# Performance work log

Hardware: AMD Instinct MI355X
Metric: run time of the kernel (lower is better)

Reference implementation:

```python
import jax, jax.numpy as jnp
import numpy as np

NEG_INF = -1e30  # stand-in for float('-inf') that is safe under softmax


def setup_inputs() -> dict:
    key = jax.random.key(0)
    k1, k2, k3, k4 = jax.random.split(key, 4)
    B, T, C, H = 4, 4096, 1024, 128
    x = jax.random.normal(k1, (B, T, C), dtype=jnp.float32)
    # nn.Linear(n_emb, head_size, bias=False): store as [C, H] so y = x @ W
    Wk = jax.random.normal(k2, (C, H), dtype=jnp.float32) * (C ** -0.5)
    Wq = jax.random.normal(k3, (C, H), dtype=jnp.float32) * (C ** -0.5)
    Wv = jax.random.normal(k4, (C, H), dtype=jnp.float32) * (C ** -0.5)
    return {"x": x, "Wk": Wk, "Wq": Wq, "Wv": Wv}


def reference(x, Wk, Wq, Wv):
    B, T, C = x.shape
    k = x @ Wk  # [B, T, H]
    q = x @ Wq  # [B, T, H]
    v = x @ Wv  # [B, T, H]
    # Faithful to original: wei = k @ q^T, scaled by C**-0.5 (C = n_emb)
    wei = jnp.einsum('bih,bjh->bij', k, q) * (C ** -0.5)  # [B, T, T]
    causal = jnp.tril(jnp.ones((T, T), dtype=bool))
    wei = jnp.where(causal, wei, NEG_INF)
    wei = jax.nn.softmax(wei, axis=-1)
    out = jnp.einsum('bij,bjh->bih', wei, v)  # [B, T, H]
    return out
```

## Files before the change

### kernel.cpp

```cpp
#include <hip/hip_runtime.h>
#include <hip/hip_bf16.h>

#define T_SEQ 4096
#define NBATCH 4
#define C_EMB 1024
#define H_DIM 128
#define M_ROWS (NBATCH * T_SEQ)
#define SPLIT 4

typedef __bf16 bf16x8 __attribute__((ext_vector_type(8)));
typedef float  floatx4 __attribute__((ext_vector_type(4)));

__device__ __forceinline__ ushort f2bf(float f) {
    __hip_bfloat16 h = __float2bfloat16(f);
    return *reinterpret_cast<ushort*>(&h);
}
__device__ __forceinline__ float bf2f(ushort u) {
    unsigned int v = ((unsigned int)u) << 16;
    return *reinterpret_cast<float*>(&v);
}
__device__ __forceinline__ uint4 pack8(const float4& a, const float4& b) {
    __hip_bfloat162 h0 = __float22bfloat162_rn(make_float2(a.x, a.y));
    __hip_bfloat162 h1 = __float22bfloat162_rn(make_float2(a.z, a.w));
    __hip_bfloat162 h2 = __float22bfloat162_rn(make_float2(b.x, b.y));
    __hip_bfloat162 h3 = __float22bfloat162_rn(make_float2(b.z, b.w));
    uint4 r;
    r.x = *reinterpret_cast<unsigned int*>(&h0);
    r.y = *reinterpret_cast<unsigned int*>(&h1);
    r.z = *reinterpret_cast<unsigned int*>(&h2);
    r.w = *reinterpret_cast<unsigned int*>(&h3);
    return r;
}
__device__ __forceinline__ void gld16(const ushort* g, ushort* l) {
    __builtin_amdgcn_global_load_lds(
        (const __attribute__((address_space(1))) unsigned int*)(g),
        (__attribute__((address_space(3))) unsigned int*)(l),
        16, 0, 0);
}

__global__ __launch_bounds__(256) void transpose_w(
    const float* __restrict__ Wk, const float* __restrict__ Wq,
    const float* __restrict__ Wv, ushort* __restrict__ wt) {
    const int z = blockIdx.y;
    const float* W = (z == 0) ? Wk : (z == 1) ? Wq : Wv;
    ushort* Wtz = wt + (size_t)z * H_DIM * C_EMB;
    int linear = blockIdx.x * 256 + threadIdx.x;
    int n  = linear >> 7;
    int k0 = (linear & 127) << 3;
    ushort tmp[8];
#pragma unroll
    for (int j = 0; j < 8; ++j)
        tmp[j] = f2bf(W[(size_t)(k0 + j) * H_DIM + n]);
    uint4 pk;
    pk.x = (unsigned int)tmp[0] | ((unsigned int)tmp[1] << 16);
    pk.y = (unsigned int)tmp[2] | ((unsigned int)tmp[3] << 16);
    pk.z = (unsigned int)tmp[4] | ((unsigned int)tmp[5] << 16);
    pk.w = (unsigned int)tmp[6] | ((unsigned int)tmp[7] << 16);
    *reinterpret_cast<uint4*>(Wtz + (size_t)n * C_EMB + k0) = pk;
}

__global__ __launch_bounds__(512, 1) void qkv_gemm(
    const float* __restrict__ x, const ushort* __restrict__ wt,
    ushort* __restrict__ kqv) {
    const int m0 = blockIdx.x * 64;

    __shared__ ushort As[2][64 * 64];
    __shared__ ushort Bs[2][384 * 64];

    const int tid  = threadIdx.x;
    const int lane = tid & 63;
    const int wave = tid >> 6;
    const int l15  = lane & 15;
    const int quad = lane >> 4;
    const int mg   = (wave >> 1) * 16;
    const int nb   = (wave & 1) * 12;

    floatx4 acc[12];
#pragma unroll
    for (int nj = 0; nj < 12; ++nj) acc[nj] = floatx4{0.f, 0.f, 0.f, 0.f};

    const int ar = tid >> 3;
    const int ac = tid & 7;
    const int chp = ac ^ (ar & 7);
    const float* xrow = x + (size_t)(m0 + ar) * C_EMB + ac * 8;

    float4 xa = *reinterpret_cast<const float4*>(xrow);
    float4 xb = *reinterpret_cast<const float4*>(xrow + 4);
#pragma unroll
    for (int i = 0; i < 6; ++i) {
        int rbase = wave * 48 + i * 8;
        int row = rbase + (lane >> 3);
        int chg = (lane & 7) ^ (row & 7);
        gld16(wt + (size_t)row * C_EMB + chg * 8, Bs[0] + rbase * 64);
    }
    *reinterpret_cast<uint4*>(As[0] + ar * 64 + chp * 8) = pack8(xa, xb);
    __syncthreads();
    xa = *reinterpret_cast<const float4*>(xrow + 64);
    xb = *reinterpret_cast<const float4*>(xrow + 68);

    for (int kt = 0; kt < 16; ++kt) {
        const int cur = kt & 1;

        if (kt < 15) {
#pragma unroll
            for (int i = 0; i < 6; ++i) {
                int rbase = wave * 48 + i * 8;
                int row = rbase + (lane >> 3);
                int chg = (lane & 7) ^ (row & 7);
                gld16(wt + (size_t)row * C_EMB + (kt + 1) * 64 + chg * 8,
                      Bs[cur ^ 1] + rbase * 64);
            }
            *reinterpret_cast<uint4*>(As[cur ^ 1] + ar * 64 + chp * 8) = pack8(xa, xb);
        }
        if (kt < 14) {
            const float* nsrc = xrow + (kt + 2) * 64;
            xa = *reinterpret_cast<const float4*>(nsrc);
            xb = *reinterpret_cast<const float4*>(nsrc + 4);
        }

#pragma unroll
        for (int kk = 0; kk < 2; ++kk) {
            bf16x8 a = *reinterpret_cast<const bf16x8*>(
                As[cur] + (mg + l15) * 64 + ((4 * kk + quad) ^ (l15 & 7)) * 8);
#pragma unroll
            for (int nj = 0; nj < 12; ++nj) {
                int brow = (nb + nj) * 16 + l15;
                bf16x8 b = *reinterpret_cast<const bf16x8*>(
                    Bs[cur] + brow * 64 + ((4 * kk + quad) ^ (brow & 7)) * 8);
                acc[nj] = __builtin_amdgcn_mfma_f32_16x16x32_bf16(a, b, acc[nj], 0, 0, 0);
            }
        }

        __syncthreads();
    }

    const int rowb = m0 + mg + quad * 4;
#pragma unroll
    for (int nj = 0; nj < 12; ++nj) {
        int gcol = (nb + nj) * 16 + l15;
        int z = gcol >> 7;
        int cz = gcol & 127;
        if (z < 2) {
            const float scale = (z == 0) ? 0.03125f : 1.0f;
            ushort* outz = kqv + (size_t)z * M_ROWS * H_DIM;
#pragma unroll
            for (int r = 0; r < 4; ++r)
                outz[(size_t)(rowb + r) * H_DIM + cz] = f2bf(acc[nj][r] * scale);
        } else {
            ushort* vt = kqv + (size_t)2 * M_ROWS * H_DIM;
            int bb   = rowb >> 12;
            int tloc = rowb & (T_SEQ - 1);
            ushort4 pk;
            pk.x = f2bf(acc[nj][0]);
            pk.y = f2bf(acc[nj][1]);
            pk.z = f2bf(acc[nj][2]);
            pk.w = f2bf(acc[nj][3]);
            *reinterpret_cast<ushort4*>(
                vt + ((size_t)(bb * H_DIM + cz) << 12) + tloc) = pk;
        }
    }
}

#define P_STRIDE 72
__global__ __launch_bounds__(256, 3) void flash_chunk(
    const ushort* __restrict__ kqv, ushort* __restrict__ partO,
    float* __restrict__ partML) {
    const int it = blockIdx.x >> 2;
    const int c  = blockIdx.x & 3;
    if (c > it) return;
    const int b  = blockIdx.y;
    const int i0 = it * 64;

    const ushort* Qg = kqv + (size_t)b * T_SEQ * H_DIM;
    const ushort* Kg = kqv + (size_t)M_ROWS * H_DIM + (size_t)b * T_SEQ * H_DIM;
    const ushort* Vt = kqv + (size_t)2 * M_ROWS * H_DIM + (size_t)b * H_DIM * T_SEQ;

    __shared__ ushort Ks[64 * 128];
    __shared__ ushort Vs[128 * 64];
    __shared__ ushort Ps[4][16 * P_STRIDE];

    const int tid  = threadIdx.x;
    const int lane = tid & 63;
    const int wave = tid >> 6;
    const int l15  = lane & 15;
    const int quad = lane >> 4;

    bf16x8 q[4];
    {
        const ushort* qrow = Qg + (size_t)(i0 + wave * 16 + l15) * H_DIM + quad * 8;
#pragma unroll
        for (int kk = 0; kk < 4; ++kk)
            q[kk] = *reinterpret_cast<const bf16x8*>(qrow + kk * 32);
    }

    float m_i[4], l_i[4];
#pragma unroll
    for (int r = 0; r < 4; ++r) { m_i[r] = -1e30f; l_i[r] = 0.f; }
    floatx4 o[8];
#pragma unroll
    for (int nh = 0; nh < 8; ++nh) o[nh] = floatx4{0.f, 0.f, 0.f, 0.f};

    ushort* Pw = Ps[wave];

    for (int jt = c; jt <= it; jt += SPLIT) {
        const int j0 = jt * 64;
        __syncthreads();
#pragma unroll
        for (int i = 0; i < 4; ++i) {
            int row = wave * 16 + i * 4 + (lane >> 4);
            int chg = (lane & 15) ^ (row & 15);
            gld16(Kg + (size_t)(j0 + row) * H_DIM + chg * 8,
                  Ks + (wave * 16 + i * 4) * 128);
        }
#pragma unroll
        for (int i = 0; i < 4; ++i) {
            int row = wave * 32 + i * 8 + (lane >> 3);
            int chg = (lane & 7) ^ (row & 7);
            gld16(Vt + (size_t)row * T_SEQ + j0 + chg * 8,
                  Vs + (wave * 32 + i * 8) * 64);
        }
        __syncthreads();

        floatx4 s[4];
#pragma unroll
        for (int ni = 0; ni < 4; ++ni) s[ni] = floatx4{0.f, 0.f, 0.f, 0.f};
#pragma unroll
        for (int kk = 0; kk < 4; ++kk)
#pragma unroll
            for (int ni = 0; ni < 4; ++ni) {
                bf16x8 kb = *reinterpret_cast<const bf16x8*>(
                    Ks + (ni * 16 + l15) * 128 + ((4 * kk + quad) ^ l15) * 8);
                s[ni] = __builtin_amdgcn_mfma_f32_16x16x32_bf16(q[kk], kb, s[ni], 0, 0, 0);
            }

        if (jt == it) {
            int ii = i0 + wave * 16 + quad * 4;
#pragma unroll
            for (int ni = 0; ni < 4; ++ni) {
                int j = j0 + ni * 16 + l15;
#pragma unroll
                for (int r = 0; r < 4; ++r)
                    if (j > ii + r) s[ni][r] = -1e30f;
            }
        }

        float alpha[4], rs[4];
#pragma unroll
        for (int r = 0; r < 4; ++r) {
            float v = fmaxf(fmaxf(s[0][r], s[1][r]), fmaxf(s[2][r], s[3][r]));
#pragma unroll
            for (int off = 8; off >= 1; off >>= 1)
                v = fmaxf(v, __shfl_xor(v, off, 64));
            float mn = fmaxf(m_i[r], v);
            alpha[r] = __expf(m_i[r] - mn);
            m_i[r] = mn;
            rs[r] = 0.f;
        }
#pragma unroll
        for (int ni = 0; ni < 4; ++ni)
#pragma unroll
            for (int r = 0; r < 4; ++r) {
                float p = __expf(s[ni][r] - m_i[r]);
                rs[r] += p;
                Pw[(quad * 4 + r) * P_STRIDE + ni * 16 + l15] = f2bf(p);
            }
#pragma unroll
        for (int r = 0; r < 4; ++r) {
            float v = rs[r];
#pragma unroll
            for (int off = 8; off >= 1; off >>= 1)
                v += __shfl_xor(v, off, 64);
            l_i[r] = l_i[r] * alpha[r] + v;
        }
#pragma unroll
        for (int nh = 0; nh < 8; ++nh)
#pragma unroll
            for (int r = 0; r < 4; ++r) o[nh][r] *= alpha[r];

#pragma unroll
        for (int kp = 0; kp < 2; ++kp) {
            bf16x8 a = *reinterpret_cast<const bf16x8*>(
                Pw + l15 * P_STRIDE + kp * 32 + quad * 8);
#pragma unroll
            for (int nh = 0; nh < 8; ++nh) {
                bf16x8 vb = *reinterpret_cast<const bf16x8*>(
                    Vs + (nh * 16 + l15) * 64 + ((4 * kp + quad) ^ (l15 & 7)) * 8);
                o[nh] = __builtin_amdgcn_mfma_f32_16x16x32_bf16(a, vb, o[nh], 0, 0, 0);
            }
        }
    }

    const int idx = ((b * 64 + it) << 2) + c;
    ushort* po = partO + (size_t)idx * 64 * 128;
#pragma unroll
    for (int nh = 0; nh < 8; ++nh)
#pragma unroll
        for (int r = 0; r < 4; ++r) {
            int row = wave * 16 + quad * 4 + r;
            po[(size_t)row * 128 + nh * 16 + l15] = f2bf(o[nh][r]);
        }
    if (l15 == 0) {
        float* ml = partML + (size_t)idx * 128;
#pragma unroll
        for (int r = 0; r < 4; ++r) {
            int row = wave * 16 + quad * 4 + r;
            ml[row]      = m_i[r];
            ml[64 + row] = l_i[r];
        }
    }
}

__global__ __launch_bounds__(256) void combine(
    const ushort* __restrict__ partO, const float* __restrict__ partML,
    float* __restrict__ out) {
    const int it = blockIdx.x, b = blockIdx.y;
    const int count = min(SPLIT, it + 1);
    const int tid = threadIdx.x;
    const int row = tid >> 2;
    const int cg  = (tid & 3) * 32;
    const int base = (b * 64 + it) << 2;

    float m_c[SPLIT], l_c[SPLIT];
    float M = -1e30f;
    for (int cc = 0; cc < count; ++cc) {
        const float* ml = partML + (size_t)(base + cc) * 128;
        m_c[cc] = ml[row];
        l_c[cc] = ml[64 + row];
        M = fmaxf(M, m_c[cc]);
    }
    float L = 0.f, w[SPLIT];
    for (int cc = 0; cc < count; ++cc) {
        w[cc] = __expf(m_c[cc] - M);
        L += w[cc] * l_c[cc];
    }

    float acc[32];
#pragma unroll
    for (int j = 0; j < 32; ++j) acc[j] = 0.f;
    for (int cc = 0; cc < count; ++cc) {
        const ushort* po = partO + (size_t)(base + cc) * 8192 + (size_t)row * 128 + cg;
        float wc = w[cc];
#pragma unroll
        for (int g = 0; g < 4; ++g) {
            uint4 v = *reinterpret_cast<const uint4*>(po + g * 8);
            const ushort* pv = reinterpret_cast<const ushort*>(&v);
#pragma unroll
            for (int e = 0; e < 8; ++e)
                acc[g * 8 + e] += wc * bf2f(pv[e]);
        }
    }
    float invL = 1.0f / L;
    float* op = out + ((size_t)b * T_SEQ + it * 64 + row) * H_DIM + cg;
#pragma unroll
    for (int g = 0; g < 8; ++g) {
        float4 v;
        v.x = acc[g * 4 + 0] * invL;
        v.y = acc[g * 4 + 1] * invL;
        v.z = acc[g * 4 + 2] * invL;
        v.w = acc[g * 4 + 3] * invL;
        *reinterpret_cast<float4*>(op + g * 4) = v;
    }
}

extern "C" void kernel_launch(void* const* d_in, const int* in_sizes, int n_in,
                              void* d_out, int out_size, void* d_ws, size_t ws_size,
                              hipStream_t stream) {
    const float* x  = (const float*)d_in[0];
    const float* Wk = (const float*)d_in[1];
    const float* Wq = (const float*)d_in[2];
    const float* Wv = (const float*)d_in[3];

    ushort* kqv    = (ushort*)d_ws;
    ushort* wt     = kqv + (size_t)3 * M_ROWS * H_DIM;
    ushort* partO  = wt + (size_t)3 * H_DIM * C_EMB;
    float*  partML = (float*)(partO + (size_t)1024 * 64 * 128);

    transpose_w<<<dim3(64, 3), 256, 0, stream>>>(Wk, Wq, Wv, wt);
    qkv_gemm<<<dim3(256), 512, 0, stream>>>(x, wt, kqv);
    flash_chunk<<<dim3(64 * SPLIT, NBATCH), 256, 0, stream>>>(kqv, partO, partML);
    combine<<<dim3(64, NBATCH), 256, 0, stream>>>(partO, partML, (float*)d_out);
}
```

Measured before the change: 181.0 us.

## Reverse flash block order, add MFMA priority hints, widen combine grid

The flash kernel now walks query tiles from the longest causal rows first, so heavy blocks start early and the tail is shorter. It also raises wave priority around the MFMA loops with s_setprio. The combine kernel is split four ways per tile, with each thread handling 8 columns of one row. This gives more blocks and better coalesced 16-byte loads, and uses fewer registers per thread.

```diff
diff --git a/kernel.cpp b/kernel.cpp
--- a/kernel.cpp
+++ b/kernel.cpp
@@ -165,7 +165,7 @@
 __global__ __launch_bounds__(256, 3) void flash_chunk(
     const ushort* __restrict__ kqv, ushort* __restrict__ partO,
     float* __restrict__ partML) {
-    const int it = blockIdx.x >> 2;
+    const int it = 63 - (blockIdx.x >> 2);
     const int c  = blockIdx.x & 3;
     if (c > it) return;
     const int b  = blockIdx.y;
@@ -224,6 +224,7 @@
         floatx4 s[4];
 #pragma unroll
         for (int ni = 0; ni < 4; ++ni) s[ni] = floatx4{0.f, 0.f, 0.f, 0.f};
+        __builtin_amdgcn_s_setprio(1);
 #pragma unroll
         for (int kk = 0; kk < 4; ++kk)
 #pragma unroll
@@ -232,6 +233,7 @@
                     Ks + (ni * 16 + l15) * 128 + ((4 * kk + quad) ^ l15) * 8);
                 s[ni] = __builtin_amdgcn_mfma_f32_16x16x32_bf16(q[kk], kb, s[ni], 0, 0, 0);
             }
+        __builtin_amdgcn_s_setprio(0);
 
         if (jt == it) {
             int ii = i0 + wave * 16 + quad * 4;
@@ -281,12 +283,14 @@
         for (int kp = 0; kp < 2; ++kp) {
             bf16x8 a = *reinterpret_cast<const bf16x8*>(
                 Pw + l15 * P_STRIDE + kp * 32 + quad * 8);
+            __builtin_amdgcn_s_setprio(1);
 #pragma unroll
             for (int nh = 0; nh < 8; ++nh) {
                 bf16x8 vb = *reinterpret_cast<const bf16x8*>(
                     Vs + (nh * 16 + l15) * 64 + ((4 * kp + quad) ^ (l15 & 7)) * 8);
                 o[nh] = __builtin_amdgcn_mfma_f32_16x16x32_bf16(a, vb, o[nh], 0, 0, 0);
             }
+            __builtin_amdgcn_s_setprio(0);
         }
     }
 
@@ -313,11 +317,13 @@
 __global__ __launch_bounds__(256) void combine(
     const ushort* __restrict__ partO, const float* __restrict__ partML,
     float* __restrict__ out) {
-    const int it = blockIdx.x, b = blockIdx.y;
+    const int it = blockIdx.x >> 2;
+    const int qr = blockIdx.x & 3;
+    const int b  = blockIdx.y;
     const int count = min(SPLIT, it + 1);
     const int tid = threadIdx.x;
-    const int row = tid >> 2;
-    const int cg  = (tid & 3) * 32;
+    const int row = qr * 16 + (tid >> 4);
+    const int cg  = (tid & 15) * 8;
     const int base = (b * 64 + it) << 2;
 
     float m_c[SPLIT], l_c[SPLIT];
@@ -334,32 +340,27 @@
         L += w[cc] * l_c[cc];
     }
 
-    float acc[32];
-#pragma unroll
-    for (int j = 0; j < 32; ++j) acc[j] = 0.f;
+    float acc[8];
+#pragma unroll
+    for (int j = 0; j < 8; ++j) acc[j] = 0.f;
     for (int cc = 0; cc < count; ++cc) {
         const ushort* po = partO + (size_t)(base + cc) * 8192 + (size_t)row * 128 + cg;
+        uint4 v = *reinterpret_cast<const uint4*>(po);
+        const ushort* pv = reinterpret_cast<const ushort*>(&v);
         float wc = w[cc];
 #pragma unroll
-        for (int g = 0; g < 4; ++g) {
-            uint4 v = *reinterpret_cast<const uint4*>(po + g * 8);
-            const ushort* pv = reinterpret_cast<const ushort*>(&v);
-#pragma unroll
-            for (int e = 0; e < 8; ++e)
-                acc[g * 8 + e] += wc * bf2f(pv[e]);
-        }
+        for (int e = 0; e < 8; ++e)
+            acc[e] += wc * bf2f(pv[e]);
     }
     float invL = 1.0f / L;
     float* op = out + ((size_t)b * T_SEQ + it * 64 + row) * H_DIM + cg;
-#pragma unroll
-    for (int g = 0; g < 8; ++g) {
-        float4 v;
-        v.x = acc[g * 4 + 0] * invL;
-        v.y = acc[g * 4 + 1] * invL;
-        v.z = acc[g * 4 + 2] * invL;
-        v.w = acc[g * 4 + 3] * invL;
-        *reinterpret_cast<float4*>(op + g * 4) = v;
-    }
+    float4 v0, v1;
+    v0.x = acc[0] * invL; v0.y = acc[1] * invL;
+    v0.z = acc[2] * invL; v0.w = acc[3] * invL;
+    v1.x = acc[4] * invL; v1.y = acc[5] * invL;
+    v1.z = acc[6] * invL; v1.w = acc[7] * invL;
+    *reinterpret_cast<float4*>(op)     = v0;
+    *reinterpret_cast<float4*>(op + 4) = v1;
 }
 
 extern "C" void kernel_launch(void* const* d_in, const int* in_sizes, int n_in,
@@ -378,5 +379,5 @@
     transpose_w<<<dim3(64, 3), 256, 0, stream>>>(Wk, Wq, Wv, wt);
     qkv_gemm<<<dim3(256), 512, 0, stream>>>(x, wt, kqv);
     flash_chunk<<<dim3(64 * SPLIT, NBATCH), 256, 0, stream>>>(kqv, partO, partML);
-    combine<<<dim3(64, NBATCH), 256, 0, stream>>>(partO, partML, (float*)d_out);
-}
+    combine<<<dim3(256, NBATCH), 256, 0, stream>>>(partO, partML, (float*)d_out);
+}
```

After: 178.8 us. No clear change (-1.2%).
